# Kernel tuning notes

Hardware: AMD Instinct MI355X
Metric: run time of the kernel (lower is better)

The kernel has to match this reference:

```python
import jax, jax.numpy as jnp
import numpy as np

B, N, C, H, HD = 32, 512, 384, 6, 64
WH = WW = WT = 8
ALPHA = 4.0
KS = 5


def safe_pow(x, p):
    # x = relu(...) >= 0; avoid nan grads at x == 0
    pos = x > 0
    return jnp.where(pos, jnp.where(pos, x, 1.0) ** p, 0.0)


def setup_inputs() -> dict:
    key = jax.random.key(0)
    ks = jax.random.split(key, 12)
    s = 0.02
    return {
        "x": jax.random.normal(ks[0], (B, N, C), jnp.float32),
        "y": jax.random.normal(ks[1], (B, N, C), jnp.float32),
        "Wqkvg": jax.random.normal(ks[2], (4 * C, C), jnp.float32) * s,
        "bqkvg": jax.random.normal(ks[3], (4 * C,), jnp.float32) * s,
        "Wproj": jax.random.normal(ks[4], (C, C), jnp.float32) * s,
        "bproj": jax.random.normal(ks[5], (C,), jnp.float32) * s,
        "dwc_w": jax.random.normal(ks[6], (HD, 1, KS, KS, KS), jnp.float32) * s,
        "dwc_b": jax.random.normal(ks[7], (HD,), jnp.float32) * s,
        "power_p": jax.random.normal(ks[8], (1, H, 1, HD), jnp.float32) * s,
        "scale_p": jax.random.normal(ks[9], (1, 1, C), jnp.float32) * s,
        "pe": jax.random.normal(ks[10], (1, N, C), jnp.float32) * s,
    }


def reference(x, y, Wqkvg, bqkvg, Wproj, bproj, dwc_w, dwc_b, power_p, scale_p, pe):
    qkv = (x @ Wqkvg.T + bqkvg).reshape(B, N, 4, C)
    k = qkv[:, :, 1]
    v = qkv[:, :, 2]
    g = qkv[:, :, 3]
    q = (y @ Wqkvg.T + bqkvg).reshape(B, N, 4, C)[:, :, 0]

    k = k + pe
    scale = jax.nn.softplus(scale_p)          # (1,1,C)
    power = 1.0 + ALPHA * jax.nn.sigmoid(power_p)  # (1,H,1,HD)
    q = q / scale
    k = k / scale

    def heads(t):  # (B,N,C) -> (B,H,N,HD)
        return t.reshape(B, N, H, HD).transpose(0, 2, 1, 3)

    q = heads(q)
    k = heads(k)
    v = heads(v)

    q_pos = safe_pow(jax.nn.relu(q), power)
    q_neg = safe_pow(jax.nn.relu(-q), power)
    k_pos = safe_pow(jax.nn.relu(k), power)
    k_neg = safe_pow(jax.nn.relu(-k), power)

    q_sim = jnp.concatenate([q_pos, q_neg], axis=-1)   # (B,H,N,2HD)
    q_opp = jnp.concatenate([q_neg, q_pos], axis=-1)
    kf = jnp.concatenate([k_pos, k_neg], axis=-1)      # (B,H,N,2HD)
    v1, v2 = jnp.split(v, 2, axis=-1)                  # each (B,H,N,HD/2)

    k_mean = kf.mean(axis=-2)                          # (B,H,2HD)
    inv_sqrt_n = N ** (-0.5)
    kfs = kf * inv_sqrt_n

    z_sim = 1.0 / (jnp.einsum("bhnd,bhd->bhn", q_sim, k_mean)[..., None] + 1e-6)
    kv1 = jnp.einsum("bhnd,bhne->bhde", kfs, v1 * inv_sqrt_n)
    x_sim = jnp.einsum("bhnd,bhde->bhne", q_sim, kv1) * z_sim

    z_opp = 1.0 / (jnp.einsum("bhnd,bhd->bhn", q_opp, k_mean)[..., None] + 1e-6)
    kv2 = jnp.einsum("bhnd,bhne->bhde", kfs, v2 * inv_sqrt_n)
    x_opp = jnp.einsum("bhnd,bhde->bhne", q_opp, kv2) * z_opp

    xa = jnp.concatenate([x_sim, x_opp], axis=-1)      # (B,H,N,HD)
    xa = xa.transpose(0, 2, 1, 3).reshape(B, N, C)

    # depthwise conv3d on v: (B*H, HD, Wh, Ww, Wt)
    vr = v.reshape(B * H, WH, WW, WT, HD).transpose(0, 4, 1, 2, 3)
    pad = KS // 2
    vc = jax.lax.conv_general_dilated(
        vr, dwc_w, window_strides=(1, 1, 1),
        padding=[(pad, pad)] * 3,
        dimension_numbers=("NCDHW", "OIDHW", "NCDHW"),
        feature_group_count=HD,
    ) + dwc_b[None, :, None, None, None]
    vc = vc.transpose(0, 2, 3, 4, 1).reshape(B, N, C)

    out = (xa + vc) * g
    out = out @ Wproj.T + bproj
    return out
```

## Files before the change

### kernel.cpp

```cpp
#include <hip/hip_runtime.h>
#include <hip/hip_bf16.h>
#include <math.h>

#define B_  32
#define N_  512
#define C_  384
#define H_  6
#define HD_ 64
#define M_  (B_*N_)

typedef __attribute__((ext_vector_type(8))) short bfrag;
typedef __attribute__((ext_vector_type(8))) unsigned short u16x8;
typedef __attribute__((ext_vector_type(4))) float f32x4;

__device__ __forceinline__ unsigned short f2bfu(float f){
  unsigned int u = __float_as_uint(f);
  u += 0x7fffu + ((u >> 16) & 1u);
  return (unsigned short)(u >> 16);
}
__device__ __forceinline__ float bf2f(unsigned short u){
  return __uint_as_float(((unsigned int)u) << 16);
}
__device__ __forceinline__ bfrag cvt8(float4 a, float4 b){
  bfrag r;
  r[0]=(short)f2bfu(a.x); r[1]=(short)f2bfu(a.y); r[2]=(short)f2bfu(a.z); r[3]=(short)f2bfu(a.w);
  r[4]=(short)f2bfu(b.x); r[5]=(short)f2bfu(b.y); r[6]=(short)f2bfu(b.z); r[7]=(short)f2bfu(b.w);
  return r;
}
__device__ __forceinline__ void gload_lds16(const unsigned short* gp, unsigned short* lp){
  __builtin_amdgcn_global_load_lds(
      (const __attribute__((address_space(1))) void*)gp,
      (__attribute__((address_space(3))) void*)lp, 16, 0, 0);
}

__global__ void param_kernel(const float* __restrict__ scale_p,
                             const float* __restrict__ power_p,
                             float* __restrict__ scale_inv,
                             float* __restrict__ power){
  int t = threadIdx.x;
  if (t < C_){
    float s  = scale_p[t];
    scale_inv[t] = 1.0f / log1pf(expf(s));
  }
  if (t < H_*HD_){
    float p = power_p[t];
    power[t] = 1.0f + 4.0f / (1.0f + expf(-p));
  }
}

__global__ void sentinel_kernel(float* __restrict__ out, int n){
  int i = blockIdx.x*256 + threadIdx.x;
  if (i < n) out[i] = 1.0e9f;
}

__global__ __launch_bounds__(256) void cvt_bf16_kernel(
    const float* __restrict__ x, const float* __restrict__ y,
    const float* __restrict__ W, const float* __restrict__ Wp,
    unsigned short* __restrict__ xb, unsigned short* __restrict__ yb,
    unsigned short* __restrict__ Wb, unsigned short* __restrict__ Wpb)
{
  const int bid = blockIdx.x;
  const float* src; unsigned short* dst; int base;
  if (bid < 3072)      { src = x;  dst = xb;  base = bid; }
  else if (bid < 6144) { src = y;  dst = yb;  base = bid - 3072; }
  else if (bid < 6432) { src = W;  dst = Wb;  base = bid - 6144; }
  else                 { src = Wp; dst = Wpb; base = bid - 6432; }
  const size_t i0 = ((size_t)base*256 + threadIdx.x)*8;
  float4 a = *reinterpret_cast<const float4*>(src + i0);
  float4 b = *reinterpret_cast<const float4*>(src + i0 + 4);
  *reinterpret_cast<bfrag*>(dst + i0) = cvt8(a, b);
}

__global__ __launch_bounds__(256,4) void gemm_qkvg(
    const unsigned short* __restrict__ xb, const unsigned short* __restrict__ yb,
    const unsigned short* __restrict__ Wb, const float* __restrict__ bias,
    const float* __restrict__ pe, const float* __restrict__ scale_inv,
    const float* __restrict__ power,
    unsigned short* __restrict__ qf, unsigned short* __restrict__ kf,
    unsigned short* __restrict__ v, unsigned short* __restrict__ g)
{
  __shared__ __align__(16) unsigned short smem[16384];

  const int tid  = threadIdx.x;
  const int bid0 = blockIdx.y * 12 + blockIdx.x;
  const int nb   = (bid0 & 7) * 192 + (bid0 >> 3);
  const int by   = nb / 12;
  const int bx   = nb - by * 12;
  const int row0 = by * 128;
  const int col0 = bx * 128;
  const int mode = bx / 3;
  const unsigned short* Ab = (mode == 0) ? yb : xb;

  const int wave = tid >> 6, lane = tid & 63;
  const int wm = (wave >> 1) * 64, wn = (wave & 1) * 64;
  const int fr = lane & 15, quad = lane >> 4;
  const int srr = tid >> 2;
  const int skc = (tid & 3) * 8;

  const unsigned short* ga0 = &Ab[(size_t)(row0 + srr)*C_ + skc];
  const unsigned short* gb0 = &Wb[(size_t)(col0 + srr)*C_ + skc];
  const size_t gstep = (size_t)64*C_;

  f32x4 acc[4][4] = {};

  gload_lds16(ga0,         &smem[tid*8]);
  gload_lds16(ga0 + gstep, &smem[2048 + tid*8]);
  gload_lds16(gb0,         &smem[8192 + tid*8]);
  gload_lds16(gb0 + gstep, &smem[8192 + 2048 + tid*8]);
  __syncthreads();

  #pragma unroll 2
  for (int t = 0; t < 12; t++){
    const int cur = t & 1;
    if (t < 11){
      const int k0 = (t+1)*32;
      const int nxt = cur^1;
      gload_lds16(ga0 + k0,         &smem[nxt*4096 + tid*8]);
      gload_lds16(ga0 + gstep + k0, &smem[nxt*4096 + 2048 + tid*8]);
      gload_lds16(gb0 + k0,         &smem[8192 + nxt*4096 + tid*8]);
      gload_lds16(gb0 + gstep + k0, &smem[8192 + nxt*4096 + 2048 + tid*8]);
    }
    bfrag af[4], bf[4];
    #pragma unroll
    for (int f = 0; f < 4; f++){
      af[f] = *reinterpret_cast<const bfrag*>(&smem[cur*4096 + (wm + f*16 + fr)*32 + quad*8]);
      bf[f] = *reinterpret_cast<const bfrag*>(&smem[8192 + cur*4096 + (wn + f*16 + fr)*32 + quad*8]);
    }
    #pragma unroll
    for (int i=0;i<4;i++)
      #pragma unroll
      for (int j=0;j<4;j++)
        acc[i][j] = __builtin_amdgcn_mfma_f32_16x16x32_bf16(af[i], bf[j], acc[i][j], 0, 0, 0);
    __syncthreads();
  }

  const int cbase = col0 - mode*384;
  if (mode <= 1){
    unsigned short* dst = (mode == 0) ? qf : kf;
    #pragma unroll
    for (int i = 0; i < 4; i++){
      const int rowb = row0 + wm + i*16 + quad*4;
      #pragma unroll
      for (int j = 0; j < 4; j++){
        const int cl = wn + j*16 + fr;
        const int cc = cbase + cl;
        const int hh = cc >> 6, dd = cc & 63;
        const float bcol = bias[mode*384 + cc];
        const float scv  = scale_inv[cc];
        const float p    = power[cc];
        #pragma unroll
        for (int r = 0; r < 4; r++){
          const int row = rowb + r;
          float val = acc[i][j][r] + bcol;
          if (mode == 1) val += pe[(row & (N_-1))*C_ + cc];
          val *= scv;
          const float ax = fabsf(val);
          const float pv = (ax > 0.0f) ? exp2f(p * log2f(ax)) : 0.0f;
          const unsigned int pos = f2bfu((val > 0.0f) ? pv : 0.0f);
          const unsigned int neg = f2bfu((val < 0.0f) ? pv : 0.0f);
          *reinterpret_cast<unsigned int*>(&dst[(size_t)row*768 + hh*128 + dd*2]) =
              pos | (neg << 16);
        }
      }
    }
  } else {
    unsigned short* dst = (mode == 2) ? v : g;
    #pragma unroll
    for (int i = 0; i < 4; i++){
      const int rowb = row0 + wm + i*16 + quad*4;
      #pragma unroll
      for (int j = 0; j < 4; j++){
        const int cc = cbase + wn + j*16 + fr;
        const float bcol = bias[mode*384 + cc];
        #pragma unroll
        for (int r = 0; r < 4; r++)
          dst[(size_t)(rowb + r)*C_ + cc] = f2bfu(acc[i][j][r] + bcol);
      }
    }
  }
}

#define NC_ 256
__global__ __launch_bounds__(512) void attn_kernel(
    const unsigned short* __restrict__ qf, const unsigned short* __restrict__ kf,
    const unsigned short* __restrict__ v, float* __restrict__ xa)
{
  const int bh = blockIdx.x;
  const int b = bh / H_, h = bh % H_;
  __shared__ __align__(16) unsigned short smem[54912];
  unsigned short* kfT  = smem;
  unsigned short* vT   = smem + 33792;
  unsigned short* kvBT = smem;

  const int tid = threadIdx.x;
  const int wave = tid >> 6, lane = tid & 63;
  const int fr = lane & 15, quad = lane >> 4;

  const unsigned short* kfg   = kf + (size_t)b*N_*768 + h*128;
  const unsigned short* vbase = v  + (size_t)b*N_*C_  + h*HD_;

  for (int i = tid; i < 16*NC_; i += 512){
    int e = 64 + (i >> 8);
    int nl = i & (NC_-1);
    vT[e*264 + nl] = (e == 64) ? (unsigned short)0x3F80 : (unsigned short)0;
  }

  auto storeA = [&](bfrag* kr, bfrag* vr){
    #pragma unroll
    for (int it = 0; it < 8; it++){
      int flat = it*512 + tid; int cg = flat & 15, nl = flat >> 4; int swz = cg << 3;
      #pragma unroll
      for (int j = 0; j < 8; j++) kfT[(cg*8+j)*264 + (nl ^ swz)] = (unsigned short)kr[it][j];
    }
    #pragma unroll
    for (int it = 0; it < 4; it++){
      int flat = it*512 + tid; int cg = flat & 7, nl = flat >> 3; int swz = cg << 3;
      #pragma unroll
      for (int j = 0; j < 8; j++) vT[(cg*8+j)*264 + (nl ^ swz)] = (unsigned short)vr[it][j];
    }
  };
  auto mfmaA = [&](f32x4* acc){
    const int arow = wave*16 + fr;
    const int aswz = (arow >> 3) << 3;
    for (int kk = 0; kk < NC_/32; kk++){
      int ko = kk*32 + quad*8;
      bfrag af = *reinterpret_cast<const bfrag*>(&kfT[arow*264 + (ko ^ aswz)]);
      #pragma unroll
      for (int j = 0; j < 5; j++){
        const int brow = j*16 + fr;
        const int bswz = (brow >> 3) << 3;
        bfrag bfr = *reinterpret_cast<const bfrag*>(&vT[brow*264 + (ko ^ bswz)]);
        acc[j] = __builtin_amdgcn_mfma_f32_16x16x32_bf16(af, bfr, acc[j], 0, 0, 0);
      }
    }
  };

  bfrag kr0[8], vr0[4], kr1[8], vr1[4];
  #pragma unroll
  for (int it = 0; it < 8; it++){ int flat = it*512 + tid; int cg = flat & 15, nl = flat >> 4;
    kr0[it] = *reinterpret_cast<const bfrag*>(&kfg[(size_t)nl*768 + cg*8]); }
  #pragma unroll
  for (int it = 0; it < 4; it++){ int flat = it*512 + tid; int cg = flat & 7, nl = flat >> 3;
    vr0[it] = *reinterpret_cast<const bfrag*>(&vbase[(size_t)nl*C_ + cg*8]); }
  storeA(kr0, vr0);
  #pragma unroll
  for (int it = 0; it < 8; it++){ int flat = it*512 + tid; int cg = flat & 15, nl = flat >> 4;
    kr1[it] = *reinterpret_cast<const bfrag*>(&kfg[(size_t)(NC_+nl)*768 + cg*8]); }
  #pragma unroll
  for (int it = 0; it < 4; it++){ int flat = it*512 + tid; int cg = flat & 7, nl = flat >> 3;
    vr1[it] = *reinterpret_cast<const bfrag*>(&vbase[(size_t)(NC_+nl)*C_ + cg*8]); }

  __syncthreads();
  f32x4 acc[5] = {};
  mfmaA(acc);
  __syncthreads();
  storeA(kr1, vr1);
  __syncthreads();
  mfmaA(acc);
  __syncthreads();

  const float invN = 1.0f / (float)N_;
  {
    const int dbase = wave*16 + quad*4;
    #pragma unroll
    for (int j = 0; j < 4; j++){
      const int e = j*16 + fr;
      const unsigned short c0 = f2bfu(acc[j][0] * invN);
      const unsigned short c1 = f2bfu(acc[j][1] * invN);
      const unsigned short c2 = f2bfu(acc[j][2] * invN);
      const unsigned short c3 = f2bfu(acc[j][3] * invN);
      ushort4 w4;
      if (e < 32){ w4.x=c0; w4.y=c1; w4.z=c2; w4.w=c3; }
      else       { w4.x=c1; w4.y=c0; w4.z=c3; w4.w=c2; }
      const int col = dbase ^ (((e >> 3) & 7) << 3);
      *reinterpret_cast<ushort4*>(&kvBT[e*136 + col]) = w4;
    }
    if (fr == 0){
      const unsigned short k0 = f2bfu(acc[4][0] * invN);
      const unsigned short k1 = f2bfu(acc[4][1] * invN);
      const unsigned short k2 = f2bfu(acc[4][2] * invN);
      const unsigned short k3 = f2bfu(acc[4][3] * invN);
      ushort4 wk;  wk.x=k0;  wk.y=k1;  wk.z=k2;  wk.w=k3;
      ushort4 wkf; wkf.x=k1; wkf.y=k0; wkf.z=k3; wkf.w=k2;
      *reinterpret_cast<ushort4*>(&kvBT[64*136 + dbase]) = wk;
      *reinterpret_cast<ushort4*>(&kvBT[65*136 + dbase]) = wkf;
    }
  }
  __syncthreads();

  const unsigned short* qfg = qf + (size_t)b*N_*768 + h*128;
  float* xabase = xa + (size_t)b*N_*C_ + h*HD_;
  const int qrow = wave*16 + fr;
  bfrag qv0[4], qv1[4];
  #pragma unroll
  for (int kk = 0; kk < 4; kk++)
    qv0[kk] = *reinterpret_cast<const bfrag*>(&qfg[(size_t)qrow*768 + kk*32 + quad*8]);

  #pragma unroll
  for (int mc = 0; mc < 4; mc++){
    bfrag* qcur = (mc & 1) ? qv1 : qv0;
    bfrag* qnxt = (mc & 1) ? qv0 : qv1;
    if (mc < 3){
      const int m1 = (mc+1) * 128;
      #pragma unroll
      for (int kk = 0; kk < 4; kk++)
        qnxt[kk] = *reinterpret_cast<const bfrag*>(&qfg[(size_t)(m1+qrow)*768 + kk*32 + quad*8]);
    }
    f32x4 a2[5] = {};
    #pragma unroll
    for (int kk = 0; kk < 4; kk++){
      int ko = kk*32 + quad*8;
      #pragma unroll
      for (int j = 0; j < 5; j++){
        const int brow = j*16 + fr;
        const int bsz = ((brow >> 3) & 7) << 3;
        bfrag bfr = *reinterpret_cast<const bfrag*>(&kvBT[brow*136 + (ko ^ bsz)]);
        a2[j] = __builtin_amdgcn_mfma_f32_16x16x32_bf16(qcur[kk], bfr, a2[j], 0, 0, 0);
      }
    }
    const int m0 = mc * 128;
    #pragma unroll
    for (int r = 0; r < 4; r++){
      const float zsim = __shfl(a2[4][r], quad*16);
      const float zopp = __shfl(a2[4][r], quad*16 + 1);
      const int n = m0 + wave*16 + quad*4 + r;
      #pragma unroll
      for (int j = 0; j < 4; j++){
        const int e = j*16 + fr;
        const float z = (e < 32) ? zsim : zopp;
        xabase[(size_t)n*C_ + e] = a2[j][r] / (z + 1e-6f);
      }
    }
  }
}

__global__ __launch_bounds__(512) void conv_kernel(
    const unsigned short* __restrict__ v, const float* __restrict__ dwc_w,
    const float* __restrict__ dwc_b, const float* __restrict__ xa,
    const unsigned short* __restrict__ g, unsigned short* __restrict__ ab)
{
  const int bh = blockIdx.x;
  const int b = bh / H_, h = bh % H_;
  const int ch0 = blockIdx.y * 16;
  __shared__ float vol[16][521];
  __shared__ float wv[16][126];
  __shared__ float wb[16];
  const int tid = threadIdx.x;
  const unsigned short* vbase = v + (size_t)b*N_*C_ + h*HD_;
  const float* xabatch = xa + (size_t)b*N_*C_ + (size_t)h*N_*HD_;
  const unsigned short* gb = g + (size_t)b*N_*C_ + (size_t)h*N_*HD_;
  unsigned short* abb = ab + (size_t)b*N_*C_ + (size_t)h*N_*HD_;

  #pragma unroll
  for (int it = 0; it < 2; it++){
    int flat = it*512 + tid;
    int co = flat & 1, n = flat >> 1;
    u16x8 v8 = *reinterpret_cast<const u16x8*>(&vbase[(size_t)n*C_ + ch0 + co*8]);
    #pragma unroll
    for (int j = 0; j < 8; j++) vol[co*8+j][n] = bf2f(v8[j]);
  }
  for (int i = tid; i < 16*125; i += 512){
    int ch = i / 125, wi = i - ch*125;
    wv[ch][wi] = dwc_w[(ch0+ch)*125 + wi];
  }
  if (tid < 16) wb[tid] = dwc_b[ch0 + tid];
  __syncthreads();

  for (int t = 0; t < 2; t++){
    const int task = t*512 + tid;
    const int ch = task & 15;
    const int zy = task >> 4;
    const int z = zy >> 3, yc = zy & 7;
    float o[8];
    const float bias = wb[ch];
    #pragma unroll
    for (int xx = 0; xx < 8; xx++) o[xx] = bias;
    #pragma unroll
    for (int kd = 0; kd < 5; kd++){
      const int zz = z + kd - 2;
      if ((unsigned)zz >= 8u) continue;
      #pragma unroll
      for (int kh = 0; kh < 5; kh++){
        const int yy = yc + kh - 2;
        if ((unsigned)yy >= 8u) continue;
        const float* row = &vol[ch][zz*64 + yy*8];
        float rr[8];
        #pragma unroll
        for (int xx = 0; xx < 8; xx++) rr[xx] = row[xx];
        const float* wrow = &wv[ch][kd*25 + kh*5];
        float w5[5];
        #pragma unroll
        for (int kw = 0; kw < 5; kw++) w5[kw] = wrow[kw];
        #pragma unroll
        for (int xx = 0; xx < 8; xx++){
          #pragma unroll
          for (int kw = 0; kw < 5; kw++){
            const int xi = xx + kw - 2;
            if ((unsigned)xi < 8u) o[xx] = fmaf(w5[kw], rr[xi], o[xx]);
          }
        }
      }
    }
    const int nb = zy * 8;
    #pragma unroll
    for (int xx = 0; xx < 8; xx++){
      const size_t di = (size_t)(nb + xx)*HD_ + ch0 + ch;
      abb[di] = f2bfu((xabatch[di] + o[xx]) * bf2f(gb[di]));
    }
  }
}

__global__ __launch_bounds__(256,4) void proj_kernel(
    const unsigned short* __restrict__ ab, const unsigned short* __restrict__ Wpb,
    const float* __restrict__ bp, float* __restrict__ out)
{
  __shared__ unsigned short As[2][4096];
  __shared__ unsigned short Bs[2][4096];

  const int tid  = threadIdx.x;
  const int bid0 = blockIdx.y * 3 + blockIdx.x;
  const int nb   = (bid0 & 7) * 48 + (bid0 >> 3);
  const int by   = nb / 3;
  const int bx   = nb - by * 3;
  const int row0 = by * 128;
  const int col0 = bx * 128;
  const int wave = tid >> 6, lane = tid & 63;
  const int wm = (wave >> 1) * 64, wn = (wave & 1) * 64;
  const int fr = lane & 15, quad = lane >> 4;
  const int srr = tid >> 2;
  const int skc = (tid & 3) * 8;

  const unsigned short* ga0 = &ab[(size_t)(row0 + srr)*C_ + skc];
  const unsigned short* gb0 = &Wpb[(size_t)(col0 + srr)*C_ + skc];
  const size_t gstep = (size_t)64*C_;

  f32x4 acc[4][4] = {};

  gload_lds16(ga0,         &As[0][tid*8]);
  gload_lds16(ga0 + gstep, &As[0][2048 + tid*8]);
  gload_lds16(gb0,         &Bs[0][tid*8]);
  gload_lds16(gb0 + gstep, &Bs[0][2048 + tid*8]);
  __syncthreads();

  #pragma unroll 2
  for (int t = 0; t < 12; t++){
    const int cur = t & 1;
    if (t < 11){
      const int k0 = (t+1)*32;
      gload_lds16(ga0 + k0,         &As[cur^1][tid*8]);
      gload_lds16(ga0 + gstep + k0, &As[cur^1][2048 + tid*8]);
      gload_lds16(gb0 + k0,         &Bs[cur^1][tid*8]);
      gload_lds16(gb0 + gstep + k0, &Bs[cur^1][2048 + tid*8]);
    }
    bfrag af[4], bf[4];
    #pragma unroll
    for (int f = 0; f < 4; f++){
      af[f] = *reinterpret_cast<const bfrag*>(&As[cur][(wm + f*16 + fr)*32 + quad*8]);
      bf[f] = *reinterpret_cast<const bfrag*>(&Bs[cur][(wn + f*16 + fr)*32 + quad*8]);
    }
    #pragma unroll
    for (int i=0;i<4;i++)
      #pragma unroll
      for (int j=0;j<4;j++)
        acc[i][j] = __builtin_amdgcn_mfma_f32_16x16x32_bf16(af[i], bf[j], acc[i][j], 0, 0, 0);
    __syncthreads();
  }

  #pragma unroll
  for (int i = 0; i < 4; i++){
    const int rowb = row0 + wm + i*16 + quad*4;
    #pragma unroll
    for (int j = 0; j < 4; j++){
      const int col = col0 + wn + j*16 + fr;
      const float bcol = bp[col];
      #pragma unroll
      for (int r = 0; r < 4; r++)
        out[(size_t)(rowb + r)*C_ + col] = acc[i][j][r] + bcol;
    }
  }
}

extern "C" void kernel_launch(void* const* d_in, const int* in_sizes, int n_in,
                              void* d_out, int out_size, void* d_ws, size_t ws_size,
                              hipStream_t stream){
  float* out = (float*)d_out;

  const int expect[11] = {6291456, 6291456, 589824, 1536, 147456, 384, 8000, 64, 384, 384, 196608};
  bool ok = (n_in == 11);
  for (int i = 0; ok && i < 11; i++) ok = (in_sizes[i] == expect[i]);
  if (!ok){
    sentinel_kernel<<<(out_size+255)/256, 256, 0, stream>>>(out, out_size);
    return;
  }

  const float* x    = (const float*)d_in[0];
  const float* y    = (const float*)d_in[1];
  const float* W    = (const float*)d_in[2];
  const float* bq   = (const float*)d_in[3];
  const float* Wp   = (const float*)d_in[4];
  const float* bp   = (const float*)d_in[5];
  const float* dwcw = (const float*)d_in[6];
  const float* dwcb = (const float*)d_in[7];
  const float* pwp  = (const float*)d_in[8];
  const float* scp  = (const float*)d_in[9];
  const float* pe   = (const float*)d_in[10];

  float* ws = (float*)d_ws;
  const size_t SZ = (size_t)M_ * C_;
  unsigned short* qf  = (unsigned short*)ws;
  unsigned short* kfb = qf + 2*SZ;
  unsigned short* v   = (unsigned short*)(ws + 2*SZ);
  unsigned short* g   = v + SZ;
  unsigned short* xb  = (unsigned short*)(ws + 3*SZ);
  unsigned short* yb  = xb + SZ;
  float* xa = ws + 3*SZ;
  unsigned short* ab  = (unsigned short*)ws;
  unsigned short* Wb  = (unsigned short*)(ws + 4*SZ);
  unsigned short* Wpb = Wb + 589824;
  float* scale_inv = (float*)(Wpb + 147456);
  float* power     = scale_inv + 512;

  param_kernel<<<1, 512, 0, stream>>>(scp, pwp, scale_inv, power);
  cvt_bf16_kernel<<<6504, 256, 0, stream>>>(x, y, W, Wp, xb, yb, Wb, Wpb);
  gemm_qkvg<<<dim3(12, 128), 256, 0, stream>>>(xb, yb, Wb, bq, pe, scale_inv, power, qf, kfb, v, g);
  attn_kernel<<<dim3(B_*H_), 512, 0, stream>>>(qf, kfb, v, xa);
  conv_kernel<<<dim3(B_*H_, 4), 512, 0, stream>>>(v, dwcw, dwcb, xa, g, ab);
  proj_kernel<<<dim3(3, 128), 256, 0, stream>>>(ab, Wpb, bp, out);
}
```

Before: 224.8 us.

## Split attention into KV-reduction and query-apply kernels for more parallelism

The single attention kernel, which ran one block per (batch, head) over all 512 queries, is split in two. The first kernel computes the kv state and k_mean and writes them to global workspace. The second kernel launches four blocks per head, each covering 128 queries, so the query phase has four times as many blocks and a smaller LDS footprint. The change adds an extra launch and a global round trip for the small kv matrix, and it also raises the occupancy hint on the two GEMM kernels from 4 to 5 blocks.

```diff
diff --git a/kernel.cpp b/kernel.cpp
--- a/kernel.cpp
+++ b/kernel.cpp
@@ -71,7 +71,7 @@
   *reinterpret_cast<bfrag*>(dst + i0) = cvt8(a, b);
 }
 
-__global__ __launch_bounds__(256,4) void gemm_qkvg(
+__global__ __launch_bounds__(256,5) void gemm_qkvg(
     const unsigned short* __restrict__ xb, const unsigned short* __restrict__ yb,
     const unsigned short* __restrict__ Wb, const float* __restrict__ bias,
     const float* __restrict__ pe, const float* __restrict__ scale_inv,
@@ -181,16 +181,15 @@
 }
 
 #define NC_ 256
-__global__ __launch_bounds__(512) void attn_kernel(
-    const unsigned short* __restrict__ qf, const unsigned short* __restrict__ kf,
-    const unsigned short* __restrict__ v, float* __restrict__ xa)
+__global__ __launch_bounds__(512) void attn_kv_kernel(
+    const unsigned short* __restrict__ kf, const unsigned short* __restrict__ v,
+    unsigned short* __restrict__ kvg)
 {
   const int bh = blockIdx.x;
   const int b = bh / H_, h = bh % H_;
   __shared__ __align__(16) unsigned short smem[54912];
   unsigned short* kfT  = smem;
   unsigned short* vT   = smem + 33792;
-  unsigned short* kvBT = smem;
 
   const int tid = threadIdx.x;
   const int wave = tid >> 6, lane = tid & 63;
@@ -257,79 +256,89 @@
   storeA(kr1, vr1);
   __syncthreads();
   mfmaA(acc);
-  __syncthreads();
 
   const float invN = 1.0f / (float)N_;
-  {
-    const int dbase = wave*16 + quad*4;
+  unsigned short* kvb = kvg + (size_t)bh * 66 * 128;
+  const int dbase = wave*16 + quad*4;
+  #pragma unroll
+  for (int j = 0; j < 4; j++){
+    const int e = j*16 + fr;
+    const unsigned short c0 = f2bfu(acc[j][0] * invN);
+    const unsigned short c1 = f2bfu(acc[j][1] * invN);
+    const unsigned short c2 = f2bfu(acc[j][2] * invN);
+    const unsigned short c3 = f2bfu(acc[j][3] * invN);
+    ushort4 w4;
+    if (e < 32){ w4.x=c0; w4.y=c1; w4.z=c2; w4.w=c3; }
+    else       { w4.x=c1; w4.y=c0; w4.z=c3; w4.w=c2; }
+    *reinterpret_cast<ushort4*>(&kvb[e*128 + dbase]) = w4;
+  }
+  if (fr == 0){
+    const unsigned short k0 = f2bfu(acc[4][0] * invN);
+    const unsigned short k1 = f2bfu(acc[4][1] * invN);
+    const unsigned short k2 = f2bfu(acc[4][2] * invN);
+    const unsigned short k3 = f2bfu(acc[4][3] * invN);
+    ushort4 wk;  wk.x=k0;  wk.y=k1;  wk.z=k2;  wk.w=k3;
+    ushort4 wkf; wkf.x=k1; wkf.y=k0; wkf.z=k3; wkf.w=k2;
+    *reinterpret_cast<ushort4*>(&kvb[64*128 + dbase]) = wk;
+    *reinterpret_cast<ushort4*>(&kvb[65*128 + dbase]) = wkf;
+  }
+}
+
+__global__ __launch_bounds__(512) void attn_qx_kernel(
+    const unsigned short* __restrict__ qf, const unsigned short* __restrict__ kvg,
+    float* __restrict__ xa)
+{
+  const int bh = blockIdx.x;
+  const int mc = blockIdx.y;
+  const int b = bh / H_, h = bh % H_;
+  __shared__ __align__(16) unsigned short kvBT[80*136];
+
+  const int tid = threadIdx.x;
+  const int wave = tid >> 6, lane = tid & 63;
+  const int fr = lane & 15, quad = lane >> 4;
+
+  const unsigned short* kvb = kvg + (size_t)bh * 66 * 128;
+  for (int i = tid; i < 80*16; i += 512){
+    const int row = i >> 4, cg = i & 15;
+    const int swz = ((row >> 3) & 7) << 3;
+    u16x8 val;
+    if (row < 66) val = *reinterpret_cast<const u16x8*>(&kvb[row*128 + cg*8]);
+    else { val[0]=0; val[1]=0; val[2]=0; val[3]=0; val[4]=0; val[5]=0; val[6]=0; val[7]=0; }
+    *reinterpret_cast<u16x8*>(&kvBT[row*136 + ((cg*8) ^ swz)]) = val;
+  }
+  __syncthreads();
+
+  const unsigned short* qfg = qf + (size_t)b*N_*768 + h*128;
+  float* xabase = xa + (size_t)b*N_*C_ + h*HD_;
+  const int m0 = mc * 128;
+  const int qrow = m0 + wave*16 + fr;
+  bfrag qv[4];
+  #pragma unroll
+  for (int kk = 0; kk < 4; kk++)
+    qv[kk] = *reinterpret_cast<const bfrag*>(&qfg[(size_t)qrow*768 + kk*32 + quad*8]);
+
+  f32x4 a2[5] = {};
+  #pragma unroll
+  for (int kk = 0; kk < 4; kk++){
+    const int ko = kk*32 + quad*8;
+    #pragma unroll
+    for (int j = 0; j < 5; j++){
+      const int brow = j*16 + fr;
+      const int bsz = ((brow >> 3) & 7) << 3;
+      bfrag bfr = *reinterpret_cast<const bfrag*>(&kvBT[brow*136 + (ko ^ bsz)]);
+      a2[j] = __builtin_amdgcn_mfma_f32_16x16x32_bf16(qv[kk], bfr, a2[j], 0, 0, 0);
+    }
+  }
+  #pragma unroll
+  for (int r = 0; r < 4; r++){
+    const float zsim = __shfl(a2[4][r], quad*16);
+    const float zopp = __shfl(a2[4][r], quad*16 + 1);
+    const int n = m0 + wave*16 + quad*4 + r;
     #pragma unroll
     for (int j = 0; j < 4; j++){
       const int e = j*16 + fr;
-      const unsigned short c0 = f2bfu(acc[j][0] * invN);
-      const unsigned short c1 = f2bfu(acc[j][1] * invN);
-      const unsigned short c2 = f2bfu(acc[j][2] * invN);
-      const unsigned short c3 = f2bfu(acc[j][3] * invN);
-      ushort4 w4;
-      if (e < 32){ w4.x=c0; w4.y=c1; w4.z=c2; w4.w=c3; }
-      else       { w4.x=c1; w4.y=c0; w4.z=c3; w4.w=c2; }
-      const int col = dbase ^ (((e >> 3) & 7) << 3);
-      *reinterpret_cast<ushort4*>(&kvBT[e*136 + col]) = w4;
-    }
-    if (fr == 0){
-      const unsigned short k0 = f2bfu(acc[4][0] * invN);
-      const unsigned short k1 = f2bfu(acc[4][1] * invN);
-      const unsigned short k2 = f2bfu(acc[4][2] * invN);
-      const unsigned short k3 = f2bfu(acc[4][3] * invN);
-      ushort4 wk;  wk.x=k0;  wk.y=k1;  wk.z=k2;  wk.w=k3;
-      ushort4 wkf; wkf.x=k1; wkf.y=k0; wkf.z=k3; wkf.w=k2;
-      *reinterpret_cast<ushort4*>(&kvBT[64*136 + dbase]) = wk;
-      *reinterpret_cast<ushort4*>(&kvBT[65*136 + dbase]) = wkf;
-    }
-  }
-  __syncthreads();
-
-  const unsigned short* qfg = qf + (size_t)b*N_*768 + h*128;
-  float* xabase = xa + (size_t)b*N_*C_ + h*HD_;
-  const int qrow = wave*16 + fr;
-  bfrag qv0[4], qv1[4];
-  #pragma unroll
-  for (int kk = 0; kk < 4; kk++)
-    qv0[kk] = *reinterpret_cast<const bfrag*>(&qfg[(size_t)qrow*768 + kk*32 + quad*8]);
-
-  #pragma unroll
-  for (int mc = 0; mc < 4; mc++){
-    bfrag* qcur = (mc & 1) ? qv1 : qv0;
-    bfrag* qnxt = (mc & 1) ? qv0 : qv1;
-    if (mc < 3){
-      const int m1 = (mc+1) * 128;
-      #pragma unroll
-      for (int kk = 0; kk < 4; kk++)
-        qnxt[kk] = *reinterpret_cast<const bfrag*>(&qfg[(size_t)(m1+qrow)*768 + kk*32 + quad*8]);
-    }
-    f32x4 a2[5] = {};
-    #pragma unroll
-    for (int kk = 0; kk < 4; kk++){
-      int ko = kk*32 + quad*8;
-      #pragma unroll
-      for (int j = 0; j < 5; j++){
-        const int brow = j*16 + fr;
-        const int bsz = ((brow >> 3) & 7) << 3;
-        bfrag bfr = *reinterpret_cast<const bfrag*>(&kvBT[brow*136 + (ko ^ bsz)]);
-        a2[j] = __builtin_amdgcn_mfma_f32_16x16x32_bf16(qcur[kk], bfr, a2[j], 0, 0, 0);
-      }
-    }
-    const int m0 = mc * 128;
-    #pragma unroll
-    for (int r = 0; r < 4; r++){
-      const float zsim = __shfl(a2[4][r], quad*16);
-      const float zopp = __shfl(a2[4][r], quad*16 + 1);
-      const int n = m0 + wave*16 + quad*4 + r;
-      #pragma unroll
-      for (int j = 0; j < 4; j++){
-        const int e = j*16 + fr;
-        const float z = (e < 32) ? zsim : zopp;
-        xabase[(size_t)n*C_ + e] = a2[j][r] / (z + 1e-6f);
-      }
+      const float z = (e < 32) ? zsim : zopp;
+      xabase[(size_t)n*C_ + e] = a2[j][r] / (z + 1e-6f);
     }
   }
 }
@@ -410,7 +419,7 @@
   }
 }
 
-__global__ __launch_bounds__(256,4) void proj_kernel(
+__global__ __launch_bounds__(256,5) void proj_kernel(
     const unsigned short* __restrict__ ab, const unsigned short* __restrict__ Wpb,
     const float* __restrict__ bp, float* __restrict__ out)
 {
@@ -519,11 +528,13 @@
   unsigned short* Wpb = Wb + 589824;
   float* scale_inv = (float*)(Wpb + 147456);
   float* power     = scale_inv + 512;
+  unsigned short* kvg = (unsigned short*)(power + 512);
 
   param_kernel<<<1, 512, 0, stream>>>(scp, pwp, scale_inv, power);
   cvt_bf16_kernel<<<6504, 256, 0, stream>>>(x, y, W, Wp, xb, yb, Wb, Wpb);
   gemm_qkvg<<<dim3(12, 128), 256, 0, stream>>>(xb, yb, Wb, bq, pe, scale_inv, power, qf, kfb, v, g);
-  attn_kernel<<<dim3(B_*H_), 512, 0, stream>>>(qf, kfb, v, xa);
+  attn_kv_kernel<<<dim3(B_*H_), 512, 0, stream>>>(kfb, v, kvg);
+  attn_qx_kernel<<<dim3(B_*H_, 4), 512, 0, stream>>>(qf, kvg, xa);
   conv_kernel<<<dim3(B_*H_, 4), 512, 0, stream>>>(v, dwcw, dwcb, xa, g, ab);
   proj_kernel<<<dim3(3, 128), 256, 0, stream>>>(ab, Wpb, bp, out);
 }
```

Measured after the change: 241.8 us. 1.08x slower.

## Load GEMM MFMA fragments directly from global memory, dropping LDS staging

Applied to the files above, without the earlier changes.

Both the QKVG and projection GEMM kernels drop the double-buffered LDS staging (global_load_lds plus barriers). Each wave now loads its bf16 fragments straight from global memory with 16-byte vector loads, and the K loop is fully unrolled. This removes LDS traffic and __syncthreads so more loads can be in flight. In exchange, each A/B tile is fetched by several waves redundantly through L1/L2 instead of being shared via LDS, and register pressure rises.

```diff
diff --git a/kernel.cpp b/kernel.cpp
--- a/kernel.cpp
+++ b/kernel.cpp
@@ -26,11 +26,6 @@
   r[0]=(short)f2bfu(a.x); r[1]=(short)f2bfu(a.y); r[2]=(short)f2bfu(a.z); r[3]=(short)f2bfu(a.w);
   r[4]=(short)f2bfu(b.x); r[5]=(short)f2bfu(b.y); r[6]=(short)f2bfu(b.z); r[7]=(short)f2bfu(b.w);
   return r;
-}
-__device__ __forceinline__ void gload_lds16(const unsigned short* gp, unsigned short* lp){
-  __builtin_amdgcn_global_load_lds(
-      (const __attribute__((address_space(1))) void*)gp,
-      (__attribute__((address_space(3))) void*)lp, 16, 0, 0);
 }
 
 __global__ void param_kernel(const float* __restrict__ scale_p,
@@ -79,8 +74,6 @@
     unsigned short* __restrict__ qf, unsigned short* __restrict__ kf,
     unsigned short* __restrict__ v, unsigned short* __restrict__ g)
 {
-  __shared__ __align__(16) unsigned short smem[16384];
-
   const int tid  = threadIdx.x;
   const int bid0 = blockIdx.y * 12 + blockIdx.x;
   const int nb   = (bid0 & 7) * 192 + (bid0 >> 3);
@@ -94,44 +87,31 @@
   const int wave = tid >> 6, lane = tid & 63;
   const int wm = (wave >> 1) * 64, wn = (wave & 1) * 64;
   const int fr = lane & 15, quad = lane >> 4;
-  const int srr = tid >> 2;
-  const int skc = (tid & 3) * 8;
-
-  const unsigned short* ga0 = &Ab[(size_t)(row0 + srr)*C_ + skc];
-  const unsigned short* gb0 = &Wb[(size_t)(col0 + srr)*C_ + skc];
-  const size_t gstep = (size_t)64*C_;
+
+  const unsigned short* arow[4];
+  const unsigned short* brow[4];
+  #pragma unroll
+  for (int f = 0; f < 4; f++){
+    arow[f] = &Ab[(size_t)(row0 + wm + f*16 + fr)*C_ + quad*8];
+    brow[f] = &Wb[(size_t)(col0 + wn + f*16 + fr)*C_ + quad*8];
+  }
 
   f32x4 acc[4][4] = {};
 
-  gload_lds16(ga0,         &smem[tid*8]);
-  gload_lds16(ga0 + gstep, &smem[2048 + tid*8]);
-  gload_lds16(gb0,         &smem[8192 + tid*8]);
-  gload_lds16(gb0 + gstep, &smem[8192 + 2048 + tid*8]);
-  __syncthreads();
-
-  #pragma unroll 2
+  #pragma unroll
   for (int t = 0; t < 12; t++){
-    const int cur = t & 1;
-    if (t < 11){
-      const int k0 = (t+1)*32;
-      const int nxt = cur^1;
-      gload_lds16(ga0 + k0,         &smem[nxt*4096 + tid*8]);
-      gload_lds16(ga0 + gstep + k0, &smem[nxt*4096 + 2048 + tid*8]);
-      gload_lds16(gb0 + k0,         &smem[8192 + nxt*4096 + tid*8]);
-      gload_lds16(gb0 + gstep + k0, &smem[8192 + nxt*4096 + 2048 + tid*8]);
-    }
+    const int k0 = t*32;
     bfrag af[4], bf[4];
     #pragma unroll
     for (int f = 0; f < 4; f++){
-      af[f] = *reinterpret_cast<const bfrag*>(&smem[cur*4096 + (wm + f*16 + fr)*32 + quad*8]);
-      bf[f] = *reinterpret_cast<const bfrag*>(&smem[8192 + cur*4096 + (wn + f*16 + fr)*32 + quad*8]);
+      af[f] = *reinterpret_cast<const bfrag*>(arow[f] + k0);
+      bf[f] = *reinterpret_cast<const bfrag*>(brow[f] + k0);
     }
     #pragma unroll
     for (int i=0;i<4;i++)
       #pragma unroll
       for (int j=0;j<4;j++)
         acc[i][j] = __builtin_amdgcn_mfma_f32_16x16x32_bf16(af[i], bf[j], acc[i][j], 0, 0, 0);
-    __syncthreads();
   }
 
   const int cbase = col0 - mode*384;
@@ -414,9 +394,6 @@
     const unsigned short* __restrict__ ab, const unsigned short* __restrict__ Wpb,
     const float* __restrict__ bp, float* __restrict__ out)
 {
-  __shared__ unsigned short As[2][4096];
-  __shared__ unsigned short Bs[2][4096];
-
   const int tid  = threadIdx.x;
   const int bid0 = blockIdx.y * 3 + blockIdx.x;
   const int nb   = (bid0 & 7) * 48 + (bid0 >> 3);
@@ -427,43 +404,31 @@
   const int wave = tid >> 6, lane = tid & 63;
   const int wm = (wave >> 1) * 64, wn = (wave & 1) * 64;
   const int fr = lane & 15, quad = lane >> 4;
-  const int srr = tid >> 2;
-  const int skc = (tid & 3) * 8;
-
-  const unsigned short* ga0 = &ab[(size_t)(row0 + srr)*C_ + skc];
-  const unsigned short* gb0 = &Wpb[(size_t)(col0 + srr)*C_ + skc];
-  const size_t gstep = (size_t)64*C_;
+
+  const unsigned short* arow[4];
+  const unsigned short* brow[4];
+  #pragma unroll
+  for (int f = 0; f < 4; f++){
+    arow[f] = &ab[(size_t)(row0 + wm + f*16 + fr)*C_ + quad*8];
+    brow[f] = &Wpb[(size_t)(col0 + wn + f*16 + fr)*C_ + quad*8];
+  }
 
   f32x4 acc[4][4] = {};
 
-  gload_lds16(ga0,         &As[0][tid*8]);
-  gload_lds16(ga0 + gstep, &As[0][2048 + tid*8]);
-  gload_lds16(gb0,         &Bs[0][tid*8]);
-  gload_lds16(gb0 + gstep, &Bs[0][2048 + tid*8]);
-  __syncthreads();
-
-  #pragma unroll 2
+  #pragma unroll
   for (int t = 0; t < 12; t++){
-    const int cur = t & 1;
-    if (t < 11){
-      const int k0 = (t+1)*32;
-      gload_lds16(ga0 + k0,         &As[cur^1][tid*8]);
-      gload_lds16(ga0 + gstep + k0, &As[cur^1][2048 + tid*8]);
-      gload_lds16(gb0 + k0,         &Bs[cur^1][tid*8]);
-      gload_lds16(gb0 + gstep + k0, &Bs[cur^1][2048 + tid*8]);
-    }
+    const int k0 = t*32;
     bfrag af[4], bf[4];
     #pragma unroll
     for (int f = 0; f < 4; f++){
-      af[f] = *reinterpret_cast<const bfrag*>(&As[cur][(wm + f*16 + fr)*32 + quad*8]);
-      bf[f] = *reinterpret_cast<const bfrag*>(&Bs[cur][(wn + f*16 + fr)*32 + quad*8]);
+      af[f] = *reinterpret_cast<const bfrag*>(arow[f] + k0);
+      bf[f] = *reinterpret_cast<const bfrag*>(brow[f] + k0);
     }
     #pragma unroll
     for (int i=0;i<4;i++)
       #pragma unroll
       for (int j=0;j<4;j++)
         acc[i][j] = __builtin_amdgcn_mfma_f32_16x16x32_bf16(af[i], bf[j], acc[i][j], 0, 0, 0);
-    __syncthreads();
   }
 
   #pragma unroll
```

Measured after the change: 287.6 us. 1.28x slower.

## Enlarge QKVG and projection GEMM tiles to 256x128 with 512 threads

Applied to the files above, without the earlier changes.

Both GEMM kernels now use 256-row by 128-column output tiles computed by 8 waves per block instead of 128x128 tiles with 4 waves. Each block loads the B (weight) tile once and shares it across twice as many rows, which halves weight-tile traffic and halves the block count. The cost is more LDS per block (48KB) and fewer blocks: only 192 for the projection GEMM, which may underfill the GPU's compute units. The epilogue indexing relies on wm from wave>>1, which extends naturally to 8 waves.

```diff
diff --git a/kernel.cpp b/kernel.cpp
--- a/kernel.cpp
+++ b/kernel.cpp
@@ -71,7 +71,7 @@
   *reinterpret_cast<bfrag*>(dst + i0) = cvt8(a, b);
 }
 
-__global__ __launch_bounds__(256,4) void gemm_qkvg(
+__global__ __launch_bounds__(512,4) void gemm_qkvg(
     const unsigned short* __restrict__ xb, const unsigned short* __restrict__ yb,
     const unsigned short* __restrict__ Wb, const float* __restrict__ bias,
     const float* __restrict__ pe, const float* __restrict__ scale_inv,
@@ -79,14 +79,14 @@
     unsigned short* __restrict__ qf, unsigned short* __restrict__ kf,
     unsigned short* __restrict__ v, unsigned short* __restrict__ g)
 {
-  __shared__ __align__(16) unsigned short smem[16384];
+  __shared__ __align__(16) unsigned short smem[24576];
 
   const int tid  = threadIdx.x;
   const int bid0 = blockIdx.y * 12 + blockIdx.x;
-  const int nb   = (bid0 & 7) * 192 + (bid0 >> 3);
+  const int nb   = (bid0 & 7) * 96 + (bid0 >> 3);
   const int by   = nb / 12;
   const int bx   = nb - by * 12;
-  const int row0 = by * 128;
+  const int row0 = by * 256;
   const int col0 = bx * 128;
   const int mode = bx / 3;
   const unsigned short* Ab = (mode == 0) ? yb : xb;
@@ -99,14 +99,13 @@
 
   const unsigned short* ga0 = &Ab[(size_t)(row0 + srr)*C_ + skc];
   const unsigned short* gb0 = &Wb[(size_t)(col0 + srr)*C_ + skc];
-  const size_t gstep = (size_t)64*C_;
+  const size_t astep = (size_t)128*C_;
 
   f32x4 acc[4][4] = {};
 
   gload_lds16(ga0,         &smem[tid*8]);
-  gload_lds16(ga0 + gstep, &smem[2048 + tid*8]);
-  gload_lds16(gb0,         &smem[8192 + tid*8]);
-  gload_lds16(gb0 + gstep, &smem[8192 + 2048 + tid*8]);
+  gload_lds16(ga0 + astep, &smem[4096 + tid*8]);
+  gload_lds16(gb0,         &smem[16384 + tid*8]);
   __syncthreads();
 
   #pragma unroll 2
@@ -115,16 +114,15 @@
     if (t < 11){
       const int k0 = (t+1)*32;
       const int nxt = cur^1;
-      gload_lds16(ga0 + k0,         &smem[nxt*4096 + tid*8]);
-      gload_lds16(ga0 + gstep + k0, &smem[nxt*4096 + 2048 + tid*8]);
-      gload_lds16(gb0 + k0,         &smem[8192 + nxt*4096 + tid*8]);
-      gload_lds16(gb0 + gstep + k0, &smem[8192 + nxt*4096 + 2048 + tid*8]);
+      gload_lds16(ga0 + k0,         &smem[nxt*8192 + tid*8]);
+      gload_lds16(ga0 + astep + k0, &smem[nxt*8192 + 4096 + tid*8]);
+      gload_lds16(gb0 + k0,         &smem[16384 + nxt*4096 + tid*8]);
     }
     bfrag af[4], bf[4];
     #pragma unroll
     for (int f = 0; f < 4; f++){
-      af[f] = *reinterpret_cast<const bfrag*>(&smem[cur*4096 + (wm + f*16 + fr)*32 + quad*8]);
-      bf[f] = *reinterpret_cast<const bfrag*>(&smem[8192 + cur*4096 + (wn + f*16 + fr)*32 + quad*8]);
+      af[f] = *reinterpret_cast<const bfrag*>(&smem[cur*8192 + (wm + f*16 + fr)*32 + quad*8]);
+      bf[f] = *reinterpret_cast<const bfrag*>(&smem[16384 + cur*4096 + (wn + f*16 + fr)*32 + quad*8]);
     }
     #pragma unroll
     for (int i=0;i<4;i++)
@@ -410,19 +408,18 @@
   }
 }
 
-__global__ __launch_bounds__(256,4) void proj_kernel(
+__global__ __launch_bounds__(512,4) void proj_kernel(
     const unsigned short* __restrict__ ab, const unsigned short* __restrict__ Wpb,
     const float* __restrict__ bp, float* __restrict__ out)
 {
-  __shared__ unsigned short As[2][4096];
-  __shared__ unsigned short Bs[2][4096];
+  __shared__ __align__(16) unsigned short smem[24576];
 
   const int tid  = threadIdx.x;
   const int bid0 = blockIdx.y * 3 + blockIdx.x;
-  const int nb   = (bid0 & 7) * 48 + (bid0 >> 3);
+  const int nb   = (bid0 & 7) * 24 + (bid0 >> 3);
   const int by   = nb / 3;
   const int bx   = nb - by * 3;
-  const int row0 = by * 128;
+  const int row0 = by * 256;
   const int col0 = bx * 128;
   const int wave = tid >> 6, lane = tid & 63;
   const int wm = (wave >> 1) * 64, wn = (wave & 1) * 64;
@@ -432,14 +429,13 @@
 
   const unsigned short* ga0 = &ab[(size_t)(row0 + srr)*C_ + skc];
   const unsigned short* gb0 = &Wpb[(size_t)(col0 + srr)*C_ + skc];
-  const size_t gstep = (size_t)64*C_;
+  const size_t astep = (size_t)128*C_;
 
   f32x4 acc[4][4] = {};
 
-  gload_lds16(ga0,         &As[0][tid*8]);
-  gload_lds16(ga0 + gstep, &As[0][2048 + tid*8]);
-  gload_lds16(gb0,         &Bs[0][tid*8]);
-  gload_lds16(gb0 + gstep, &Bs[0][2048 + tid*8]);
+  gload_lds16(ga0,         &smem[tid*8]);
+  gload_lds16(ga0 + astep, &smem[4096 + tid*8]);
+  gload_lds16(gb0,         &smem[16384 + tid*8]);
   __syncthreads();
 
   #pragma unroll 2
@@ -447,16 +443,16 @@
     const int cur = t & 1;
     if (t < 11){
       const int k0 = (t+1)*32;
-      gload_lds16(ga0 + k0,         &As[cur^1][tid*8]);
-      gload_lds16(ga0 + gstep + k0, &As[cur^1][2048 + tid*8]);
-      gload_lds16(gb0 + k0,         &Bs[cur^1][tid*8]);
-      gload_lds16(gb0 + gstep + k0, &Bs[cur^1][2048 + tid*8]);
+      const int nxt = cur^1;
+      gload_lds16(ga0 + k0,         &smem[nxt*8192 + tid*8]);
+      gload_lds16(ga0 + astep + k0, &smem[nxt*8192 + 4096 + tid*8]);
+      gload_lds16(gb0 + k0,         &smem[16384 + nxt*4096 + tid*8]);
     }
     bfrag af[4], bf[4];
     #pragma unroll
     for (int f = 0; f < 4; f++){
-      af[f] = *reinterpret_cast<const bfrag*>(&As[cur][(wm + f*16 + fr)*32 + quad*8]);
-      bf[f] = *reinterpret_cast<const bfrag*>(&Bs[cur][(wn + f*16 + fr)*32 + quad*8]);
+      af[f] = *reinterpret_cast<const bfrag*>(&smem[cur*8192 + (wm + f*16 + fr)*32 + quad*8]);
+      bf[f] = *reinterpret_cast<const bfrag*>(&smem[16384 + cur*4096 + (wn + f*16 + fr)*32 + quad*8]);
     }
     #pragma unroll
     for (int i=0;i<4;i++)
@@ -522,8 +518,8 @@
 
   param_kernel<<<1, 512, 0, stream>>>(scp, pwp, scale_inv, power);
   cvt_bf16_kernel<<<6504, 256, 0, stream>>>(x, y, W, Wp, xb, yb, Wb, Wpb);
-  gemm_qkvg<<<dim3(12, 128), 256, 0, stream>>>(xb, yb, Wb, bq, pe, scale_inv, power, qf, kfb, v, g);
+  gemm_qkvg<<<dim3(12, 64), 512, 0, stream>>>(xb, yb, Wb, bq, pe, scale_inv, power, qf, kfb, v, g);
   attn_kernel<<<dim3(B_*H_), 512, 0, stream>>>(qf, kfb, v, xa);
   conv_kernel<<<dim3(B_*H_, 4), 512, 0, stream>>>(v, dwcw, dwcb, xa, g, ab);
-  proj_kernel<<<dim3(3, 128), 256, 0, stream>>>(ab, Wpb, bp, out);
-}
+  proj_kernel<<<dim3(3, 64), 512, 0, stream>>>(ab, Wpb, bp, out);
+}
```

Result: no change. 227.0 us (+0.9%).
